# Performance work log

Hardware: AMD Instinct MI355X
Metric: run time of the kernel (lower is better)

## Reference

```python
import jax, jax.numpy as jnp
import numpy as np

B, L, D = 8, 512, 512
VOCAB = 50257
N_CLASSES = 225          # ceil(sqrt(50257))
N_PER_CLASS = 224        # ceil(50257 / 225)


def _glorot(key, shape, fan_in, fan_out):
    s = np.sqrt(6.0 / (fan_in + fan_out)).astype(np.float32)
    return jax.random.uniform(key, shape, jnp.float32, -s, s)


def setup_inputs() -> dict:
    key = jax.random.key(0)
    k = jax.random.split(key, 4)
    x = jax.random.normal(k[0], (B, L, D), jnp.float32)
    target = jax.random.randint(k[1], (B, L), 0, VOCAB)
    W1 = _glorot(k[2], (D, N_CLASSES), D, N_CLASSES)
    b1 = jnp.zeros((N_CLASSES,), jnp.float32)
    W2 = _glorot(k[3], (N_CLASSES, D, N_PER_CLASS), D, N_PER_CLASS)
    b2 = jnp.zeros((N_CLASSES, N_PER_CLASS), jnp.float32)
    return {"x": x, "target": target, "W1": W1, "b1": b1, "W2": W2, "b2": b2}


def reference(x, target, W1, b1, W2, b2):
    # Theano h_softmax with target given: returns p(target | x), shape [B, L, 1].
    xf = x.reshape(-1, D)                      # [N, D]
    t = target.reshape(-1)                     # [N]
    cls = t // N_PER_CLASS                     # class id per token
    idx = t % N_PER_CLASS                      # within-class id per token

    class_p = jax.nn.softmax(xf @ W1 + b1, axis=-1)          # [N, C]

    W2g = W2[cls]                                            # gather: [N, D, O]
    in_logits = jnp.einsum('nd,ndo->no', xf, W2g) + b2[cls]  # [N, O]
    in_p = jax.nn.softmax(in_logits, axis=-1)                # [N, O]

    n = jnp.arange(xf.shape[0])
    p = class_p[n, cls] * in_p[n, idx]                       # [N]
    return p.reshape(B, L, 1)
```

## Files before the change

### kernel.cpp

```cpp
#include <hip/hip_runtime.h>
#include <cmath>

typedef _Float16 half8 __attribute__((ext_vector_type(8)));
typedef float f32x4 __attribute__((ext_vector_type(4)));

constexpr int D   = 512;
constexpr int NC  = 225;
constexpr int NPC = 224;
constexpr int N1  = 256;
constexpr int TB  = 32;

constexpr int WS_NCHUNK = 0;
constexpr int WS_CHUNK  = 16;
constexpr int WS_ORDER  = 4096;
constexpr int WS_B1P    = 8192;
constexpr int WS_W1H    = 8448;
constexpr int WS_W1L    = 73984;
constexpr int WS_XH     = 139520;
constexpr int WS_XL     = 1188096;
constexpr int WS_STAT   = 2236672;

__device__ __forceinline__ void f16split(float v, _Float16& h, _Float16& l) {
    _Float16 hh = (_Float16)v;
    float hf = (float)hh;
    if (fabsf(hf) < 6.104e-5f) { hh = (_Float16)0.f; hf = 0.f; }
    h = hh;
    l = (_Float16)((v - hf) * 2048.0f);
}

__global__ __launch_bounds__(256) void k_prep_pre(
    const float* __restrict__ x, const float* __restrict__ W1,
    const float* __restrict__ b1, const int* __restrict__ target,
    int* __restrict__ ws, int ntok)
{
    const int bid = blockIdx.x, tid = threadIdx.x;
    if (bid == 0) {
        __shared__ int h[256], sc[256], sc2[256], cur[NC];
        h[tid] = 0;
        __syncthreads();
        for (int n = tid; n < ntok; n += 256) atomicAdd(&h[target[n] / NPC], 1);
        __syncthreads();
        const int hv = h[tid];
        sc[tid] = hv; __syncthreads();
        for (int o = 1; o < 256; o <<= 1) {
            int a = (tid >= o) ? sc[tid - o] : 0;
            __syncthreads();
            sc[tid] += a;
            __syncthreads();
        }
        const int start = sc[tid] - hv;
        const int nch = (tid < NC) ? (hv + TB - 1) / TB : 0;
        sc2[tid] = nch; __syncthreads();
        for (int o = 1; o < 256; o <<= 1) {
            int a = (tid >= o) ? sc2[tid - o] : 0;
            __syncthreads();
            sc2[tid] += a;
            __syncthreads();
        }
        const int nch2 = sc2[255];
        if (tid < NC) {
            cur[tid] = start;
            const int cb = sc2[tid] - nch;
            for (int j = 0; j < nch; ++j) {
                for (int q = 0; q < 2; ++q) {
                    const int e = WS_CHUNK + (((cb + j) * 2) + q) * 4;
                    ws[e + 0] = tid;
                    ws[e + 1] = start + j * TB;
                    ws[e + 2] = min(TB, hv - j * TB);
                    ws[e + 3] = q;
                }
            }
        }
        const int P1C = ntok / TB;
        if (tid < P1C) {
            for (int q = 0; q < 2; ++q) {
                const int e = WS_CHUNK + (nch2 * 2 + tid * 2 + q) * 4;
                ws[e + 0] = -1;
                ws[e + 1] = tid * TB;
                ws[e + 2] = TB;
                ws[e + 3] = q;
            }
        }
        if (tid == 0) ws[WS_NCHUNK] = nch2 * 2 + P1C * 2;
        __syncthreads();
        for (int n = tid; n < ntok; n += 256) {
            const int c = target[n] / NPC;
            const int pos = atomicAdd(&cur[c], 1);
            ws[WS_ORDER + pos] = n;
        }
        return;
    }
    const int pb = bid - 1;
    _Float16* xh  = (_Float16*)(ws + WS_XH);
    _Float16* xl  = (_Float16*)(ws + WS_XL);
    _Float16* w1h = (_Float16*)(ws + WS_W1H);
    _Float16* w1l = (_Float16*)(ws + WS_W1L);
    const int XBLK = (ntok * D) / (256 * 8);
    if (pb < XBLK) {
        const int base = (pb * 256 + tid) * 8;
        const float4 a = *(const float4*)(x + base);
        const float4 b = *(const float4*)(x + base + 4);
        const float v[8] = {a.x, a.y, a.z, a.w, b.x, b.y, b.z, b.w};
        half8 hv, lv;
        #pragma unroll
        for (int j = 0; j < 8; ++j) {
            _Float16 hq, lq;
            f16split(v[j], hq, lq);
            hv[j] = hq; lv[j] = lq;
        }
        *(half8*)(xh + base) = hv;
        *(half8*)(xl + base) = lv;
    } else if (pb < XBLK + 64) {
        const int oi = ((pb - XBLK) * 256 + tid) * 8;
        const int c = oi >> 9, k0 = oi & 511;
        half8 hv, lv;
        #pragma unroll
        for (int j = 0; j < 8; ++j) {
            const float v = (c < NC) ? W1[(size_t)(k0 + j) * NC + c] : 0.f;
            _Float16 hq, lq;
            f16split(v, hq, lq);
            hv[j] = hq; lv[j] = lq;
        }
        *(half8*)(w1h + oi) = hv;
        *(half8*)(w1l + oi) = lv;
    } else {
        float* b1p = (float*)ws + WS_B1P;
        if (tid < N1) b1p[tid] = (tid < NC) ? b1[tid] : 0.f;
    }
}

#define LX(bh, bl, kk)                                                           \
    do {                                                                         \
        _Pragma("unroll")                                                        \
        for (int n = 0; n < 2; ++n) if (n < ntiles) {                            \
            bh[n] = *(const half8*)(xh + xoff[n] + (kk) + l4 * 8);               \
            bl[n] = *(const half8*)(xl + xoff[n] + (kk) + l4 * 8);               \
        }                                                                        \
    } while (0)

#define LA(ah, al, kk)                                                           \
    do {                                                                         \
        _Pragma("unroll")                                                        \
        for (int mi = 0; mi < 2; ++mi) if (tval[mi]) {                           \
            const int col_ = (mt0 + mi) * 16 + l15;                              \
            ah[mi] = *(const half8*)(w1h + (size_t)col_ * D + (kk) + l4 * 8);    \
            al[mi] = *(const half8*)(w1l + (size_t)col_ * D + (kk) + l4 * 8);    \
        }                                                                        \
    } while (0)

#define PROCA(ah, al, bh, bl)                                                    \
    do {                                                                         \
        _Pragma("unroll")                                                        \
        for (int mi = 0; mi < 2; ++mi) if (tval[mi]) {                           \
            _Pragma("unroll")                                                    \
            for (int n = 0; n < 2; ++n) if (n < ntiles) {                        \
                accA[mi][n] = __builtin_amdgcn_mfma_f32_16x16x32_f16(ah[mi], bh[n], accA[mi][n], 0, 0, 0); \
                accB[mi][n] = __builtin_amdgcn_mfma_f32_16x16x32_f16(ah[mi], bl[n], accB[mi][n], 0, 0, 0); \
                accB[mi][n] = __builtin_amdgcn_mfma_f32_16x16x32_f16(al[mi], bh[n], accB[mi][n], 0, 0, 0); \
            }                                                                    \
        }                                                                        \
    } while (0)

__device__ __forceinline__ void run_p2(
    const int* __restrict__ target, const float* __restrict__ W2c,
    const float* __restrict__ bsrc,
    const _Float16* __restrict__ xh, const _Float16* __restrict__ xl,
    int* __restrict__ ws, int* __restrict__ stok, float* __restrict__ wtile,
    int start, int cnt, int ch)
{
    const int tid = threadIdx.x, w = tid >> 6, lane = tid & 63;
    const int l15 = lane & 15, l4 = lane >> 4;

    if (tid < TB) stok[tid] = ws[WS_ORDER + start + min(tid, cnt - 1)];
    __syncthreads();

    const int ntiles = (cnt + 15) >> 4;
    int xoff[2];
    xoff[0] = stok[l15] * D;
    xoff[1] = stok[16 + l15] * D;

    const int lt0 = w * 2;
    bool tval[2];
    tval[0] = (lt0 < 7);
    tval[1] = (lt0 + 1 < 7);

    f32x4 accA[2][2] = {}, accB[2][2] = {};

    const char* gW = (const char*)W2c + ch * 448;

    #define STAGE(buf, kt)                                                          \
        do {                                                                        \
            const char* gb_ = gW + (size_t)(kt) * 28672;                            \
            _Pragma("unroll")                                                       \
            for (int i_ = 0; i_ < 4; ++i_) {                                        \
                const int ii_ = w + i_ * 4;                                         \
                if (ii_ < 14) {                                                     \
                    const int flat_ = ii_ * 1024 + lane * 16;                       \
                    const int row_ = flat_ / 448, off_ = flat_ % 448;               \
                    __builtin_amdgcn_global_load_lds(                               \
                        (const __attribute__((address_space(1))) uint32_t*)         \
                            (gb_ + (size_t)row_ * 896 + off_),                      \
                        (__attribute__((address_space(3))) uint32_t*)               \
                            (wtile + (buf) * 3584 + ii_ * 256),                     \
                        16, 0, 0);                                                  \
                }                                                                   \
            }                                                                       \
        } while (0)

    STAGE(0, 0);
    __syncthreads();

    for (int kt = 0; kt < 16; ++kt) {
        const int cur = kt & 1;
        if (kt + 1 < 16) STAGE(cur ^ 1, kt + 1);
        const int k0 = kt * 32;
        half8 Bh[2], Bl[2];
        LX(Bh, Bl, k0);
        #pragma unroll
        for (int mi = 0; mi < 2; ++mi) if (tval[mi]) {
            half8 Ah, Al;
            const float* wrow = wtile + cur * 3584 + (lt0 + mi) * 16 + l15;
            #pragma unroll
            for (int j = 0; j < 8; ++j) {
                _Float16 hq, lq;
                f16split(wrow[(l4 * 8 + j) * 112], hq, lq);
                Ah[j] = hq; Al[j] = lq;
            }
            #pragma unroll
            for (int n = 0; n < 2; ++n) if (n < ntiles) {
                accA[mi][n] = __builtin_amdgcn_mfma_f32_16x16x32_f16(Ah, Bh[n], accA[mi][n], 0, 0, 0);
                accB[mi][n] = __builtin_amdgcn_mfma_f32_16x16x32_f16(Ah, Bl[n], accB[mi][n], 0, 0, 0);
                accB[mi][n] = __builtin_amdgcn_mfma_f32_16x16x32_f16(Al, Bh[n], accB[mi][n], 0, 0, 0);
            }
        }
        __syncthreads();
    }
    #undef STAGE

    float* stat = (float*)ws + WS_STAT;
    #pragma unroll
    for (int n = 0; n < 2; ++n) {
        if (n < ntiles) {
            const int tok = stok[n * 16 + l15];
            const int tcol = target[tok] % NPC;
            float vals[2][4];
            float mx = -1e30f;
            #pragma unroll
            for (int mi = 0; mi < 2; ++mi) if (tval[mi]) {
                const int col0 = (ch * 7 + lt0 + mi) * 16 + l4 * 4;
                const float4 bv = *(const float4*)(bsrc + col0);
                #pragma unroll
                for (int r = 0; r < 4; ++r) {
                    const float v = accA[mi][n][r] + accB[mi][n][r] * (1.f / 2048.f) + (&bv.x)[r];
                    vals[mi][r] = v;
                    mx = fmaxf(mx, v);
                }
            }
            mx = fmaxf(mx, __shfl_xor(mx, 16, 64));
            mx = fmaxf(mx, __shfl_xor(mx, 32, 64));
            float s = 0.f, e = 0.f;
            #pragma unroll
            for (int mi = 0; mi < 2; ++mi) if (tval[mi]) {
                const int col0 = (ch * 7 + lt0 + mi) * 16 + l4 * 4;
                #pragma unroll
                for (int r = 0; r < 4; ++r) {
                    const float ex = __expf(vals[mi][r] - mx);
                    s += ex;
                    if (col0 + r == tcol) e = ex;
                }
            }
            s += __shfl_xor(s, 16, 64); s += __shfl_xor(s, 32, 64);
            e += __shfl_xor(e, 16, 64); e += __shfl_xor(e, 32, 64);
            if (l4 == 0) {
                const int g = 8 + ch * 4 + w;
                *(float4*)(stat + (size_t)tok * 64 + g * 4) = {mx, s, e, 0.f};
            }
        }
    }
}

__device__ __forceinline__ void run_p1(
    const int* __restrict__ target, const float* __restrict__ bsrc,
    const _Float16* __restrict__ w1h, const _Float16* __restrict__ w1l,
    const _Float16* __restrict__ xh, const _Float16* __restrict__ xl,
    int* __restrict__ ws, int* __restrict__ stok,
    int start, int cnt, int ch)
{
    constexpr int NREAL = NC;
    const int tid = threadIdx.x, w = tid >> 6, lane = tid & 63;
    const int l15 = lane & 15, l4 = lane >> 4;

    if (tid < TB) stok[tid] = start + tid;
    __syncthreads();

    const int ntiles = 2;
    int xoff[2];
    xoff[0] = stok[l15] * D;
    xoff[1] = stok[16 + l15] * D;

    const int mt0 = ch * 8 + w * 2;
    bool tval[2];
    tval[0] = (mt0 * 16) < NREAL;
    tval[1] = ((mt0 + 1) * 16) < NREAL;

    f32x4 accA[2][2] = {}, accB[2][2] = {};

    half8 aha[2], ala[2], ahb[2], alb[2];
    half8 xha[2], xla[2], xhb[2], xlb[2];
    LA(aha, ala, 0); LX(xha, xla, 0);
    for (int k0 = 0; k0 < D; k0 += 64) {
        LA(ahb, alb, k0 + 32); LX(xhb, xlb, k0 + 32);
        PROCA(aha, ala, xha, xla);
        if (k0 + 64 < D) { LA(aha, ala, k0 + 64); LX(xha, xla, k0 + 64); }
        PROCA(ahb, alb, xhb, xlb);
    }

    float* stat = (float*)ws + WS_STAT;
    #pragma unroll
    for (int n = 0; n < 2; ++n) {
        const int tok = stok[n * 16 + l15];
        const int tcol = target[tok] / NPC;
        float vals[2][4];
        float mx = -1e30f;
        #pragma unroll
        for (int mi = 0; mi < 2; ++mi) {
            const int col0 = (mt0 + mi) * 16 + l4 * 4;
            const float4 bv = *(const float4*)(bsrc + col0);
            #pragma unroll
            for (int r = 0; r < 4; ++r) {
                const float v = accA[mi][n][r] + accB[mi][n][r] * (1.f / 2048.f) + (&bv.x)[r];
                vals[mi][r] = v;
                if (col0 + r < NREAL) mx = fmaxf(mx, v);
            }
        }
        mx = fmaxf(mx, __shfl_xor(mx, 16, 64));
        mx = fmaxf(mx, __shfl_xor(mx, 32, 64));
        float s = 0.f, e = 0.f;
        #pragma unroll
        for (int mi = 0; mi < 2; ++mi) {
            const int col0 = (mt0 + mi) * 16 + l4 * 4;
            #pragma unroll
            for (int r = 0; r < 4; ++r) {
                const int cr = col0 + r;
                if (cr < NREAL) {
                    const float ex = __expf(vals[mi][r] - mx);
                    s += ex;
                    if (cr == tcol) e = ex;
                }
            }
        }
        s += __shfl_xor(s, 16, 64); s += __shfl_xor(s, 32, 64);
        e += __shfl_xor(e, 16, 64); e += __shfl_xor(e, 32, 64);
        if (l4 == 0) {
            const int g = ch * 4 + w;
            *(float4*)(stat + (size_t)tok * 64 + g * 4) = {mx, s, e, 0.f};
        }
    }
}

__global__ __launch_bounds__(256, 4) void k_main(
    const int* __restrict__ target, const float* __restrict__ W2,
    const float* __restrict__ b2, int* __restrict__ ws)
{
    __shared__ float wtile[2 * 3584];
    __shared__ int stok[TB];
    const int bid = blockIdx.x;
    if (bid >= ws[WS_NCHUNK]) return;
    const int4 ce = *(const int4*)(ws + WS_CHUNK + bid * 4);
    const _Float16* w1h = (const _Float16*)(ws + WS_W1H);
    const _Float16* w1l = (const _Float16*)(ws + WS_W1L);
    const _Float16* xh  = (const _Float16*)(ws + WS_XH);
    const _Float16* xl  = (const _Float16*)(ws + WS_XL);
    if (ce.x >= 0) {
        run_p2(target, W2 + (size_t)ce.x * D * NPC, b2 + ce.x * NPC,
               xh, xl, ws, stok, wtile, ce.y, ce.z, ce.w);
    } else {
        run_p1(target, (const float*)ws + WS_B1P, w1h, w1l,
               xh, xl, ws, stok, ce.y, ce.z, ce.w);
    }
}

__global__ __launch_bounds__(256) void k_combine(const int* __restrict__ ws,
                                                 float* __restrict__ out, int ntok) {
    const int n = blockIdx.x * 256 + threadIdx.x;
    if (n >= ntok) return;
    const float4* st = (const float4*)((const float*)ws + WS_STAT) + (size_t)n * 16;
    float p[2];
    #pragma unroll
    for (int ph = 0; ph < 2; ++ph) {
        float M = -1e30f;
        #pragma unroll
        for (int g = 0; g < 8; ++g) M = fmaxf(M, st[ph * 8 + g].x);
        float S = 0.f, E = 0.f;
        #pragma unroll
        for (int g = 0; g < 8; ++g) {
            const float4 q = st[ph * 8 + g];
            const float sc = __expf(q.x - M);
            S += q.y * sc;
            E += q.z * sc;
        }
        p[ph] = E / S;
    }
    out[n] = p[0] * p[1];
}

extern "C" void kernel_launch(void* const* d_in, const int* in_sizes, int n_in,
                              void* d_out, int out_size, void* d_ws, size_t ws_size,
                              hipStream_t stream) {
    const float* x      = (const float*)d_in[0];
    const int*   target = (const int*)  d_in[1];
    const float* W1     = (const float*)d_in[2];
    const float* b1     = (const float*)d_in[3];
    const float* W2     = (const float*)d_in[4];
    const float* b2     = (const float*)d_in[5];
    float* out = (float*)d_out;
    int*   wsi = (int*)d_ws;

    const int ntok = in_sizes[1];
    const int maxgrid = 2 * (NC + ntok / TB) + 2 * (ntok / TB);
    const int pregrid = 1 + (ntok * D) / (256 * 8) + 64 + 1;

    k_prep_pre<<<pregrid, 256, 0, stream>>>(x, W1, b1, target, wsi, ntok);
    k_main    <<<maxgrid, 256, 0, stream>>>(target, W2, b2, wsi);
    k_combine <<<(ntok + 255) / 256, 256, 0, stream>>>(wsi, out, ntok);
}
```

Baseline: 54.95 us.

## Stage x tiles through LDS with async loads and unify phase kernels

Activation fragments (hi/lo f16 split of x) are now fetched with global_load_lds into a double-buffered LDS tile shared by all waves, instead of each wave loading them directly from global memory. Both phases run through one templated chunk routine, so the class-softmax phase also gets the LDS double-buffering and per-k-step sync, while its W1 fragments stay as direct global loads. This aims to cut redundant global traffic for x and overlap its fetch with MFMA work. In exchange it adds LDS usage and barriers, and phase 1 loses its previous register-level software prefetch.

```diff
diff --git a/kernel.cpp b/kernel.cpp
--- a/kernel.cpp
+++ b/kernel.cpp
@@ -129,66 +129,45 @@
     }
 }
 
-#define LX(bh, bl, kk)                                                           \
-    do {                                                                         \
-        _Pragma("unroll")                                                        \
-        for (int n = 0; n < 2; ++n) if (n < ntiles) {                            \
-            bh[n] = *(const half8*)(xh + xoff[n] + (kk) + l4 * 8);               \
-            bl[n] = *(const half8*)(xl + xoff[n] + (kk) + l4 * 8);               \
-        }                                                                        \
-    } while (0)
-
-#define LA(ah, al, kk)                                                           \
-    do {                                                                         \
-        _Pragma("unroll")                                                        \
-        for (int mi = 0; mi < 2; ++mi) if (tval[mi]) {                           \
-            const int col_ = (mt0 + mi) * 16 + l15;                              \
-            ah[mi] = *(const half8*)(w1h + (size_t)col_ * D + (kk) + l4 * 8);    \
-            al[mi] = *(const half8*)(w1l + (size_t)col_ * D + (kk) + l4 * 8);    \
-        }                                                                        \
-    } while (0)
-
-#define PROCA(ah, al, bh, bl)                                                    \
-    do {                                                                         \
-        _Pragma("unroll")                                                        \
-        for (int mi = 0; mi < 2; ++mi) if (tval[mi]) {                           \
-            _Pragma("unroll")                                                    \
-            for (int n = 0; n < 2; ++n) if (n < ntiles) {                        \
-                accA[mi][n] = __builtin_amdgcn_mfma_f32_16x16x32_f16(ah[mi], bh[n], accA[mi][n], 0, 0, 0); \
-                accB[mi][n] = __builtin_amdgcn_mfma_f32_16x16x32_f16(ah[mi], bl[n], accB[mi][n], 0, 0, 0); \
-                accB[mi][n] = __builtin_amdgcn_mfma_f32_16x16x32_f16(al[mi], bh[n], accB[mi][n], 0, 0, 0); \
-            }                                                                    \
-        }                                                                        \
-    } while (0)
-
-__device__ __forceinline__ void run_p2(
+template <bool PH2>
+__device__ __forceinline__ void run_chunk(
     const int* __restrict__ target, const float* __restrict__ W2c,
     const float* __restrict__ bsrc,
-    const _Float16* __restrict__ xh, const _Float16* __restrict__ xl,
-    int* __restrict__ ws, int* __restrict__ stok, float* __restrict__ wtile,
+    const _Float16* __restrict__ w1h, const _Float16* __restrict__ w1l,
+    const _Float16* __restrict__ xh_g, const _Float16* __restrict__ xl_g,
+    int* __restrict__ ws, int* __restrict__ stok,
+    float* __restrict__ wtile, _Float16* __restrict__ xtile,
     int start, int cnt, int ch)
 {
+    constexpr int NREAL = PH2 ? NPC : NC;
     const int tid = threadIdx.x, w = tid >> 6, lane = tid & 63;
     const int l15 = lane & 15, l4 = lane >> 4;
 
-    if (tid < TB) stok[tid] = ws[WS_ORDER + start + min(tid, cnt - 1)];
+    if (tid < TB)
+        stok[tid] = PH2 ? ws[WS_ORDER + start + min(tid, cnt - 1)] : (start + tid);
     __syncthreads();
 
-    const int ntiles = (cnt + 15) >> 4;
-    int xoff[2];
-    xoff[0] = stok[l15] * D;
-    xoff[1] = stok[16 + l15] * D;
-
-    const int lt0 = w * 2;
+    const int ntiles = PH2 ? ((cnt + 15) >> 4) : 2;
+    const int mt0 = PH2 ? (w * 2) : (ch * 8 + w * 2);
     bool tval[2];
-    tval[0] = (lt0 < 7);
-    tval[1] = (lt0 + 1 < 7);
-
-    f32x4 accA[2][2] = {}, accB[2][2] = {};
-
-    const char* gW = (const char*)W2c + ch * 448;
-
-    #define STAGE(buf, kt)                                                          \
+    if (PH2) { tval[0] = (mt0 < 7); tval[1] = (mt0 + 1 < 7); }
+    else     { tval[0] = (mt0 * 16) < NREAL; tval[1] = ((mt0 + 1) * 16) < NREAL; }
+
+    const int part = w >> 1, halfsel = w & 1;
+    const int xtok = stok[halfsel * 16 + (lane >> 2)];
+    const size_t xsrcoff = (size_t)xtok * 1024 + (size_t)(lane & 3) * 16;
+    const char* xsrc = part ? (const char*)xl_g : (const char*)xh_g;
+    const char* gW = PH2 ? ((const char*)W2c + ch * 448) : nullptr;
+
+    #define STAGE_X(buf, kt)                                                        \
+        __builtin_amdgcn_global_load_lds(                                           \
+            (const __attribute__((address_space(1))) uint32_t*)                     \
+                (xsrc + xsrcoff + (size_t)(kt) * 64),                               \
+            (__attribute__((address_space(3))) uint32_t*)                           \
+                ((char*)xtile + (buf) * 4096 + part * 2048 + halfsel * 1024),       \
+            16, 0, 0)
+
+    #define STAGE_W(buf, kt)                                                        \
         do {                                                                        \
             const char* gb_ = gW + (size_t)(kt) * 28672;                            \
             _Pragma("unroll")                                                       \
@@ -207,24 +186,41 @@
             }                                                                       \
         } while (0)
 
-    STAGE(0, 0);
+    f32x4 accA[2][2] = {}, accB[2][2] = {};
+
+    if (PH2) STAGE_W(0, 0);
+    STAGE_X(0, 0);
     __syncthreads();
 
     for (int kt = 0; kt < 16; ++kt) {
         const int cur = kt & 1;
-        if (kt + 1 < 16) STAGE(cur ^ 1, kt + 1);
-        const int k0 = kt * 32;
+        if (kt + 1 < 16) {
+            if (PH2) STAGE_W(cur ^ 1, kt + 1);
+            STAGE_X(cur ^ 1, kt + 1);
+        }
+        const char* xb = (const char*)xtile + cur * 4096;
         half8 Bh[2], Bl[2];
-        LX(Bh, Bl, k0);
+        #pragma unroll
+        for (int n = 0; n < 2; ++n) if (n < ntiles) {
+            Bh[n] = *(const half8*)(xb + (n * 16 + l15) * 64 + l4 * 16);
+            Bl[n] = *(const half8*)(xb + 2048 + (n * 16 + l15) * 64 + l4 * 16);
+        }
         #pragma unroll
         for (int mi = 0; mi < 2; ++mi) if (tval[mi]) {
             half8 Ah, Al;
-            const float* wrow = wtile + cur * 3584 + (lt0 + mi) * 16 + l15;
-            #pragma unroll
-            for (int j = 0; j < 8; ++j) {
-                _Float16 hq, lq;
-                f16split(wrow[(l4 * 8 + j) * 112], hq, lq);
-                Ah[j] = hq; Al[j] = lq;
+            if (PH2) {
+                const float* wrow = wtile + cur * 3584 + (mt0 + mi) * 16 + l15;
+                #pragma unroll
+                for (int j = 0; j < 8; ++j) {
+                    _Float16 hq, lq;
+                    f16split(wrow[(l4 * 8 + j) * 112], hq, lq);
+                    Ah[j] = hq; Al[j] = lq;
+                }
+            } else {
+                const int col = (mt0 + mi) * 16 + l15;
+                const int k0 = kt * 32;
+                Ah = *(const half8*)(w1h + (size_t)col * D + k0 + l4 * 8);
+                Al = *(const half8*)(w1l + (size_t)col * D + k0 + l4 * 8);
             }
             #pragma unroll
             for (int n = 0; n < 2; ++n) if (n < ntiles) {
@@ -235,25 +231,28 @@
         }
         __syncthreads();
     }
-    #undef STAGE
+    #undef STAGE_W
+    #undef STAGE_X
 
     float* stat = (float*)ws + WS_STAT;
     #pragma unroll
     for (int n = 0; n < 2; ++n) {
         if (n < ntiles) {
             const int tok = stok[n * 16 + l15];
-            const int tcol = target[tok] % NPC;
+            const int tt  = target[tok];
+            const int tcol = PH2 ? (tt % NPC) : (tt / NPC);
             float vals[2][4];
             float mx = -1e30f;
             #pragma unroll
             for (int mi = 0; mi < 2; ++mi) if (tval[mi]) {
-                const int col0 = (ch * 7 + lt0 + mi) * 16 + l4 * 4;
+                const int col0 = PH2 ? ((ch * 7 + mt0 + mi) * 16 + l4 * 4)
+                                     : ((mt0 + mi) * 16 + l4 * 4);
                 const float4 bv = *(const float4*)(bsrc + col0);
                 #pragma unroll
                 for (int r = 0; r < 4; ++r) {
                     const float v = accA[mi][n][r] + accB[mi][n][r] * (1.f / 2048.f) + (&bv.x)[r];
                     vals[mi][r] = v;
-                    mx = fmaxf(mx, v);
+                    if (col0 + r < NREAL) mx = fmaxf(mx, v);
                 }
             }
             mx = fmaxf(mx, __shfl_xor(mx, 16, 64));
@@ -261,99 +260,24 @@
             float s = 0.f, e = 0.f;
             #pragma unroll
             for (int mi = 0; mi < 2; ++mi) if (tval[mi]) {
-                const int col0 = (ch * 7 + lt0 + mi) * 16 + l4 * 4;
+                const int col0 = PH2 ? ((ch * 7 + mt0 + mi) * 16 + l4 * 4)
+                                     : ((mt0 + mi) * 16 + l4 * 4);
                 #pragma unroll
                 for (int r = 0; r < 4; ++r) {
-                    const float ex = __expf(vals[mi][r] - mx);
-                    s += ex;
-                    if (col0 + r == tcol) e = ex;
+                    const int cr = col0 + r;
+                    if (cr < NREAL) {
+                        const float ex = __expf(vals[mi][r] - mx);
+                        s += ex;
+                        if (cr == tcol) e = ex;
+                    }
                 }
             }
             s += __shfl_xor(s, 16, 64); s += __shfl_xor(s, 32, 64);
             e += __shfl_xor(e, 16, 64); e += __shfl_xor(e, 32, 64);
             if (l4 == 0) {
-                const int g = 8 + ch * 4 + w;
+                const int g = (PH2 ? 8 : 0) + ch * 4 + w;
                 *(float4*)(stat + (size_t)tok * 64 + g * 4) = {mx, s, e, 0.f};
             }
-        }
-    }
-}
-
-__device__ __forceinline__ void run_p1(
-    const int* __restrict__ target, const float* __restrict__ bsrc,
-    const _Float16* __restrict__ w1h, const _Float16* __restrict__ w1l,
-    const _Float16* __restrict__ xh, const _Float16* __restrict__ xl,
-    int* __restrict__ ws, int* __restrict__ stok,
-    int start, int cnt, int ch)
-{
-    constexpr int NREAL = NC;
-    const int tid = threadIdx.x, w = tid >> 6, lane = tid & 63;
-    const int l15 = lane & 15, l4 = lane >> 4;
-
-    if (tid < TB) stok[tid] = start + tid;
-    __syncthreads();
-
-    const int ntiles = 2;
-    int xoff[2];
-    xoff[0] = stok[l15] * D;
-    xoff[1] = stok[16 + l15] * D;
-
-    const int mt0 = ch * 8 + w * 2;
-    bool tval[2];
-    tval[0] = (mt0 * 16) < NREAL;
-    tval[1] = ((mt0 + 1) * 16) < NREAL;
-
-    f32x4 accA[2][2] = {}, accB[2][2] = {};
-
-    half8 aha[2], ala[2], ahb[2], alb[2];
-    half8 xha[2], xla[2], xhb[2], xlb[2];
-    LA(aha, ala, 0); LX(xha, xla, 0);
-    for (int k0 = 0; k0 < D; k0 += 64) {
-        LA(ahb, alb, k0 + 32); LX(xhb, xlb, k0 + 32);
-        PROCA(aha, ala, xha, xla);
-        if (k0 + 64 < D) { LA(aha, ala, k0 + 64); LX(xha, xla, k0 + 64); }
-        PROCA(ahb, alb, xhb, xlb);
-    }
-
-    float* stat = (float*)ws + WS_STAT;
-    #pragma unroll
-    for (int n = 0; n < 2; ++n) {
-        const int tok = stok[n * 16 + l15];
-        const int tcol = target[tok] / NPC;
-        float vals[2][4];
-        float mx = -1e30f;
-        #pragma unroll
-        for (int mi = 0; mi < 2; ++mi) {
-            const int col0 = (mt0 + mi) * 16 + l4 * 4;
-            const float4 bv = *(const float4*)(bsrc + col0);
-            #pragma unroll
-            for (int r = 0; r < 4; ++r) {
-                const float v = accA[mi][n][r] + accB[mi][n][r] * (1.f / 2048.f) + (&bv.x)[r];
-                vals[mi][r] = v;
-                if (col0 + r < NREAL) mx = fmaxf(mx, v);
-            }
-        }
-        mx = fmaxf(mx, __shfl_xor(mx, 16, 64));
-        mx = fmaxf(mx, __shfl_xor(mx, 32, 64));
-        float s = 0.f, e = 0.f;
-        #pragma unroll
-        for (int mi = 0; mi < 2; ++mi) {
-            const int col0 = (mt0 + mi) * 16 + l4 * 4;
-            #pragma unroll
-            for (int r = 0; r < 4; ++r) {
-                const int cr = col0 + r;
-                if (cr < NREAL) {
-                    const float ex = __expf(vals[mi][r] - mx);
-                    s += ex;
-                    if (cr == tcol) e = ex;
-                }
-            }
-        }
-        s += __shfl_xor(s, 16, 64); s += __shfl_xor(s, 32, 64);
-        e += __shfl_xor(e, 16, 64); e += __shfl_xor(e, 32, 64);
-        if (l4 == 0) {
-            const int g = ch * 4 + w;
-            *(float4*)(stat + (size_t)tok * 64 + g * 4) = {mx, s, e, 0.f};
         }
     }
 }
@@ -363,6 +287,7 @@
     const float* __restrict__ b2, int* __restrict__ ws)
 {
     __shared__ float wtile[2 * 3584];
+    __shared__ _Float16 xtile[2 * 2048];
     __shared__ int stok[TB];
     const int bid = blockIdx.x;
     if (bid >= ws[WS_NCHUNK]) return;
@@ -372,11 +297,11 @@
     const _Float16* xh  = (const _Float16*)(ws + WS_XH);
     const _Float16* xl  = (const _Float16*)(ws + WS_XL);
     if (ce.x >= 0) {
-        run_p2(target, W2 + (size_t)ce.x * D * NPC, b2 + ce.x * NPC,
-               xh, xl, ws, stok, wtile, ce.y, ce.z, ce.w);
+        run_chunk<true>(target, W2 + (size_t)ce.x * D * NPC, b2 + ce.x * NPC,
+                        w1h, w1l, xh, xl, ws, stok, wtile, xtile, ce.y, ce.z, ce.w);
     } else {
-        run_p1(target, (const float*)ws + WS_B1P, w1h, w1l,
-               xh, xl, ws, stok, ce.y, ce.z, ce.w);
+        run_chunk<false>(target, nullptr, (const float*)ws + WS_B1P,
+                         w1h, w1l, xh, xl, ws, stok, wtile, xtile, ce.y, ce.z, ce.w);
     }
 }
 
```

Result: faster. 47.98 us, median of 2 (-12.7%).
